# Performance work log

Measured on AMD Instinct MI355X. Metric: run time of the kernel, lower is better.

The kernel has to match this reference:

```python
import jax, jax.numpy as jnp
import numpy as np

LATENT_H = 5
LATENT_W = 5
BN_EPS = 1e-5


def setup_inputs() -> dict:
    key = jax.random.key(0)
    k1, k2 = jax.random.split(key)
    B, T, C, H, W = 8, 4, 512, 32, 32
    return {
        "left_features": jax.random.normal(k1, (B, T, C, H, W), dtype=jnp.float32),
        "right_features": jax.random.normal(k2, (B, T, C, H, W), dtype=jnp.float32),
        "bn_gamma": jnp.ones((C,), dtype=jnp.float32),
        "bn_beta": jnp.zeros((C,), dtype=jnp.float32),
    }


def _batchnorm_per_t(x, gamma, beta):
    # x: (B, T, C, H, W); train-mode BN applied independently at each timestep
    # (stats over batch + spatial dims, per channel, per t)
    mu = jnp.mean(x, axis=(0, 3, 4), keepdims=True)          # (1, T, C, 1, 1)
    var = jnp.var(x, axis=(0, 3, 4), keepdims=True)
    g = gamma[None, None, :, None, None]
    b = beta[None, None, :, None, None]
    return (x - mu) * jax.lax.rsqrt(var + BN_EPS) * g + b


def reference(left_features, right_features, bn_gamma, bn_beta):
    l = _batchnorm_per_t(left_features, bn_gamma, bn_beta)
    r = _batchnorm_per_t(right_features, bn_gamma, bn_beta)
    # channel-summed squared difference: (B, T, H, W)
    diff2 = jnp.sum((l - r) ** 2, axis=2)
    # latent_h x latent_w windowed mean, stride 1, VALID -> (B, T, Hp, Wp)
    win_sum = jax.lax.reduce_window(
        diff2, 0.0, jax.lax.add,
        window_dimensions=(1, 1, LATENT_H, LATENT_W),
        window_strides=(1, 1, 1, 1),
        padding="VALID",
    )
    heatmap = jnp.sqrt(win_sum / (LATENT_H * LATENT_W))
    B, T, Hp, Wp = heatmap.shape
    flat = heatmap.reshape(B, T, Hp * Wp)
    asymmetry_values = jnp.max(flat, axis=-1)                # (B, T)
    idx = jnp.argmin(flat, axis=-1)                          # (B, T)
    x_argmin = idx % Wp
    y_argmin = idx // Wp
    asymmetry_coords = jnp.stack([x_argmin, y_argmin], axis=-1)  # (B, T, 2)
    return asymmetry_values, asymmetry_coords, heatmap
```

## Files before the change

### kernel.cpp

```cpp
#include <hip/hip_runtime.h>

#define T_ 4
#define C_ 512
#define B_ 8
#define HW_ 1024
#define W_ 32
#define HP_ 28
#define EPS_ 1e-5f
#define CCH 16
#define NCHUNK (C_ / CCH)

__global__ __launch_bounds__(256) void stats_kernel(const float* __restrict__ L,
                                                    const float* __restrict__ R,
                                                    const float* __restrict__ gamma,
                                                    float4* __restrict__ coef) {
    const int tc = blockIdx.x;
    const int tid = threadIdx.x;
    const int t = tc >> 9;
    const int c = tc & (C_ - 1);
    const float4* L4 = (const float4*)L;
    const float4* R4 = (const float4*)R;

    float sl = 0.f, ql = 0.f, sr = 0.f, qr = 0.f;
#pragma unroll
    for (int b = 0; b < B_; ++b) {
        size_t base4 = ((size_t)(b * T_ + t) * C_ + c) * (HW_ / 4);
        float4 vl = L4[base4 + tid];
        float4 vr = R4[base4 + tid];
        sl += vl.x + vl.y + vl.z + vl.w;
        ql += vl.x * vl.x + vl.y * vl.y + vl.z * vl.z + vl.w * vl.w;
        sr += vr.x + vr.y + vr.z + vr.w;
        qr += vr.x * vr.x + vr.y * vr.y + vr.z * vr.z + vr.w * vr.w;
    }

#pragma unroll
    for (int off = 32; off > 0; off >>= 1) {
        sl += __shfl_down(sl, off);
        ql += __shfl_down(ql, off);
        sr += __shfl_down(sr, off);
        qr += __shfl_down(qr, off);
    }

    __shared__ float red[4][4];
    const int wave = tid >> 6, lane = tid & 63;
    if (lane == 0) {
        red[0][wave] = sl; red[1][wave] = ql;
        red[2][wave] = sr; red[3][wave] = qr;
    }
    __syncthreads();
    if (tid == 0) {
        float S  = red[0][0] + red[0][1] + red[0][2] + red[0][3];
        float Q  = red[1][0] + red[1][1] + red[1][2] + red[1][3];
        float Sr = red[2][0] + red[2][1] + red[2][2] + red[2][3];
        float Qr = red[3][0] + red[3][1] + red[3][2] + red[3][3];
        const float inv = 1.0f / (float)(B_ * HW_);
        float mul = S * inv, mur = Sr * inv;
        float varl = Q * inv - mul * mul;
        float varr = Qr * inv - mur * mur;
        float s_l = rsqrtf(varl + EPS_);
        float s_r = rsqrtf(varr + EPS_);
        float g = gamma[c];
        coef[tc] = make_float4(g * s_l, g * s_r, g * (s_l * mul - s_r * mur), 0.f);
    }
}

__global__ __launch_bounds__(256) void diff2_kernel(const float* __restrict__ L,
                                                    const float* __restrict__ R,
                                                    const float4* __restrict__ coef,
                                                    float4* __restrict__ part4) {
    const int chunk = blockIdx.x;
    const int bt = blockIdx.y;
    const int t = bt & (T_ - 1);
    const int tid = threadIdx.x;
    const int c0 = chunk * CCH;

    __shared__ float4 cf[CCH];
    if (tid < CCH) cf[tid] = coef[t * C_ + c0 + tid];
    __syncthreads();

    const float4* L4 = (const float4*)L;
    const float4* R4 = (const float4*)R;
    const size_t base4 = ((size_t)bt * C_ + c0) * (HW_ / 4);

    float a0 = 0.f, a1 = 0.f, a2 = 0.f, a3 = 0.f;
#pragma unroll
    for (int cc = 0; cc < CCH; ++cc) {
        float4 k = cf[cc];
        float4 vl = L4[base4 + cc * (HW_ / 4) + tid];
        float4 vr = R4[base4 + cc * (HW_ / 4) + tid];
        float d0 = k.x * vl.x - k.y * vr.x - k.z;
        float d1 = k.x * vl.y - k.y * vr.y - k.z;
        float d2 = k.x * vl.z - k.y * vr.z - k.z;
        float d3 = k.x * vl.w - k.y * vr.w - k.z;
        a0 += d0 * d0; a1 += d1 * d1; a2 += d2 * d2; a3 += d3 * d3;
    }
    part4[((size_t)chunk * (B_ * T_) + bt) * (HW_ / 4) + tid] =
        make_float4(a0, a1, a2, a3);
}

__global__ __launch_bounds__(256) void finalize_kernel(const float4* __restrict__ part4,
                                                       float* __restrict__ out) {
    const int bt = blockIdx.x;
    const int tid = threadIdx.x;
    __shared__ float d[HW_];
    __shared__ float rowsum[32][HP_];
    __shared__ float rv[256];
    __shared__ int   ri[256];
    __shared__ float rmax[256];

    float4 s = make_float4(0.f, 0.f, 0.f, 0.f);
#pragma unroll
    for (int ch = 0; ch < NCHUNK; ++ch) {
        float4 v = part4[((size_t)ch * (B_ * T_) + bt) * (HW_ / 4) + tid];
        s.x += v.x; s.y += v.y; s.z += v.z; s.w += v.w;
    }
    ((float4*)d)[tid] = s;
    __syncthreads();

    for (int i = tid; i < 32 * HP_; i += 256) {
        int h = i / HP_, w = i % HP_;
        const float* row = d + h * W_ + w;
        rowsum[h][w] = row[0] + row[1] + row[2] + row[3] + row[4];
    }
    __syncthreads();

    float lmax = -1e30f, lmin = 1e30f;
    int lidx = 0;
    for (int i = tid; i < HP_ * HP_; i += 256) {
        int hh = i / HP_, w = i % HP_;
        float ws = rowsum[hh][w] + rowsum[hh + 1][w] + rowsum[hh + 2][w] +
                   rowsum[hh + 3][w] + rowsum[hh + 4][w];
        float hm = sqrtf(ws * (1.0f / 25.0f));
        out[96 + (size_t)bt * (HP_ * HP_) + i] = hm;
        lmax = fmaxf(lmax, hm);
        if (hm < lmin) { lmin = hm; lidx = i; }
    }
    rv[tid] = lmin; ri[tid] = lidx; rmax[tid] = lmax;
    __syncthreads();
    for (int st = 128; st > 0; st >>= 1) {
        if (tid < st) {
            float ov = rv[tid + st]; int oi = ri[tid + st];
            if (ov < rv[tid] || (ov == rv[tid] && oi < ri[tid])) { rv[tid] = ov; ri[tid] = oi; }
            rmax[tid] = fmaxf(rmax[tid], rmax[tid + st]);
        }
        __syncthreads();
    }
    if (tid == 0) {
        out[bt] = rmax[0];
        int idx = ri[0];
        out[32 + 2 * bt + 0] = (float)(idx % HP_);
        out[32 + 2 * bt + 1] = (float)(idx / HP_);
    }
}

extern "C" void kernel_launch(void* const* d_in, const int* in_sizes, int n_in,
                              void* d_out, int out_size, void* d_ws, size_t ws_size,
                              hipStream_t stream) {
    const float* L = (const float*)d_in[0];
    const float* R = (const float*)d_in[1];
    const float* gamma = (const float*)d_in[2];
    float* out = (float*)d_out;

    float4* coef = (float4*)d_ws;
    float4* part4 = (float4*)((char*)d_ws + 4 * sizeof(float4) * (T_ * C_) / 4 * 4);
    part4 = (float4*)((char*)d_ws + sizeof(float4) * (T_ * C_));

    stats_kernel<<<T_ * C_, 256, 0, stream>>>(L, R, gamma, coef);
    diff2_kernel<<<dim3(NCHUNK, B_ * T_), 256, 0, stream>>>(L, R, coef, part4);
    finalize_kernel<<<B_ * T_, 256, 0, stream>>>(part4, out);
}
```

Baseline: 171.4 us.

## Split BN stats per row into wave-level partials and fold finalize into diff2

The stats kernel now assigns one wave to each (b,t,c) row and writes per-row partial sums, replacing one block per (t,c) that strided across the batch. The diff2 kernel reduces those partials over the batch and computes the BN coefficients in shared memory before its main loop. That main loop is also unrolled by four channels so more loads are in flight. The aim is contiguous per-wave memory access and more loads in flight for these bandwidth-bound passes, in exchange for a small redundant coefficient computation in every diff2 block.

```diff
diff --git a/kernel.cpp b/kernel.cpp
--- a/kernel.cpp
+++ b/kernel.cpp
@@ -9,29 +9,40 @@
 #define EPS_ 1e-5f
 #define CCH 16
 #define NCHUNK (C_ / CCH)
+#define NBT (B_ * T_)
+#define NROWS (B_ * T_ * C_)
 
 __global__ __launch_bounds__(256) void stats_kernel(const float* __restrict__ L,
                                                     const float* __restrict__ R,
-                                                    const float* __restrict__ gamma,
-                                                    float4* __restrict__ coef) {
-    const int tc = blockIdx.x;
-    const int tid = threadIdx.x;
-    const int t = tc >> 9;
-    const int c = tc & (C_ - 1);
+                                                    float4* __restrict__ part_s) {
+    const int wave = threadIdx.x >> 6;
+    const int lane = threadIdx.x & 63;
+    const int row = blockIdx.x * 4 + wave;
     const float4* L4 = (const float4*)L;
     const float4* R4 = (const float4*)R;
-
-    float sl = 0.f, ql = 0.f, sr = 0.f, qr = 0.f;
-#pragma unroll
-    for (int b = 0; b < B_; ++b) {
-        size_t base4 = ((size_t)(b * T_ + t) * C_ + c) * (HW_ / 4);
-        float4 vl = L4[base4 + tid];
-        float4 vr = R4[base4 + tid];
-        sl += vl.x + vl.y + vl.z + vl.w;
-        ql += vl.x * vl.x + vl.y * vl.y + vl.z * vl.z + vl.w * vl.w;
-        sr += vr.x + vr.y + vr.z + vr.w;
-        qr += vr.x * vr.x + vr.y * vr.y + vr.z * vr.z + vr.w * vr.w;
-    }
+    const size_t base = (size_t)row * 256 + lane;
+
+    float4 l0 = L4[base      ];
+    float4 l1 = L4[base +  64];
+    float4 l2 = L4[base + 128];
+    float4 l3 = L4[base + 192];
+    float4 r0 = R4[base      ];
+    float4 r1 = R4[base +  64];
+    float4 r2 = R4[base + 128];
+    float4 r3 = R4[base + 192];
+
+    float sl = (l0.x + l0.y + l0.z + l0.w) + (l1.x + l1.y + l1.z + l1.w)
+             + (l2.x + l2.y + l2.z + l2.w) + (l3.x + l3.y + l3.z + l3.w);
+    float ql = (l0.x*l0.x + l0.y*l0.y + l0.z*l0.z + l0.w*l0.w)
+             + (l1.x*l1.x + l1.y*l1.y + l1.z*l1.z + l1.w*l1.w)
+             + (l2.x*l2.x + l2.y*l2.y + l2.z*l2.z + l2.w*l2.w)
+             + (l3.x*l3.x + l3.y*l3.y + l3.z*l3.z + l3.w*l3.w);
+    float sr = (r0.x + r0.y + r0.z + r0.w) + (r1.x + r1.y + r1.z + r1.w)
+             + (r2.x + r2.y + r2.z + r2.w) + (r3.x + r3.y + r3.z + r3.w);
+    float qr = (r0.x*r0.x + r0.y*r0.y + r0.z*r0.z + r0.w*r0.w)
+             + (r1.x*r1.x + r1.y*r1.y + r1.z*r1.z + r1.w*r1.w)
+             + (r2.x*r2.x + r2.y*r2.y + r2.z*r2.z + r2.w*r2.w)
+             + (r3.x*r3.x + r3.y*r3.y + r3.z*r3.z + r3.w*r3.w);
 
 #pragma unroll
     for (int off = 32; off > 0; off >>= 1) {
@@ -40,42 +51,44 @@
         sr += __shfl_down(sr, off);
         qr += __shfl_down(qr, off);
     }
-
-    __shared__ float red[4][4];
-    const int wave = tid >> 6, lane = tid & 63;
-    if (lane == 0) {
-        red[0][wave] = sl; red[1][wave] = ql;
-        red[2][wave] = sr; red[3][wave] = qr;
-    }
-    __syncthreads();
-    if (tid == 0) {
-        float S  = red[0][0] + red[0][1] + red[0][2] + red[0][3];
-        float Q  = red[1][0] + red[1][1] + red[1][2] + red[1][3];
-        float Sr = red[2][0] + red[2][1] + red[2][2] + red[2][3];
-        float Qr = red[3][0] + red[3][1] + red[3][2] + red[3][3];
+    if (lane == 0) part_s[row] = make_float4(sl, ql, sr, qr);
+}
+
+__global__ __launch_bounds__(256) void diff2_kernel(const float* __restrict__ L,
+                                                    const float* __restrict__ R,
+                                                    const float4* __restrict__ part_s,
+                                                    const float* __restrict__ gamma,
+                                                    float4* __restrict__ part4) {
+    const int chunk = blockIdx.x;
+    const int bt = blockIdx.y;
+    const int t = bt & (T_ - 1);
+    const int tid = threadIdx.x;
+    const int c0 = chunk * CCH;
+
+    __shared__ float4 spart[B_][CCH];
+    __shared__ float4 cf[CCH];
+
+    if (tid < B_ * CCH) {
+        int bg = tid >> 4, ci = tid & (CCH - 1);
+        spart[bg][ci] = part_s[(bg * T_ + t) * C_ + c0 + ci];
+    }
+    __syncthreads();
+    if (tid < CCH) {
+        float S = 0.f, Q = 0.f, Sr = 0.f, Qr = 0.f;
+#pragma unroll
+        for (int bg = 0; bg < B_; ++bg) {
+            float4 v = spart[bg][tid];
+            S += v.x; Q += v.y; Sr += v.z; Qr += v.w;
+        }
         const float inv = 1.0f / (float)(B_ * HW_);
         float mul = S * inv, mur = Sr * inv;
         float varl = Q * inv - mul * mul;
         float varr = Qr * inv - mur * mur;
         float s_l = rsqrtf(varl + EPS_);
         float s_r = rsqrtf(varr + EPS_);
-        float g = gamma[c];
-        coef[tc] = make_float4(g * s_l, g * s_r, g * (s_l * mul - s_r * mur), 0.f);
-    }
-}
-
-__global__ __launch_bounds__(256) void diff2_kernel(const float* __restrict__ L,
-                                                    const float* __restrict__ R,
-                                                    const float4* __restrict__ coef,
-                                                    float4* __restrict__ part4) {
-    const int chunk = blockIdx.x;
-    const int bt = blockIdx.y;
-    const int t = bt & (T_ - 1);
-    const int tid = threadIdx.x;
-    const int c0 = chunk * CCH;
-
-    __shared__ float4 cf[CCH];
-    if (tid < CCH) cf[tid] = coef[t * C_ + c0 + tid];
+        float g = gamma[c0 + tid];
+        cf[tid] = make_float4(g * s_l, g * s_r, g * (s_l * mul - s_r * mur), 0.f);
+    }
     __syncthreads();
 
     const float4* L4 = (const float4*)L;
@@ -84,18 +97,35 @@
 
     float a0 = 0.f, a1 = 0.f, a2 = 0.f, a3 = 0.f;
 #pragma unroll
-    for (int cc = 0; cc < CCH; ++cc) {
-        float4 k = cf[cc];
-        float4 vl = L4[base4 + cc * (HW_ / 4) + tid];
-        float4 vr = R4[base4 + cc * (HW_ / 4) + tid];
-        float d0 = k.x * vl.x - k.y * vr.x - k.z;
-        float d1 = k.x * vl.y - k.y * vr.y - k.z;
-        float d2 = k.x * vl.z - k.y * vr.z - k.z;
-        float d3 = k.x * vl.w - k.y * vr.w - k.z;
-        a0 += d0 * d0; a1 += d1 * d1; a2 += d2 * d2; a3 += d3 * d3;
-    }
-    part4[((size_t)chunk * (B_ * T_) + bt) * (HW_ / 4) + tid] =
-        make_float4(a0, a1, a2, a3);
+    for (int cc = 0; cc < CCH; cc += 4) {
+        float4 vl0 = L4[base4 + (cc + 0) * (HW_ / 4) + tid];
+        float4 vl1 = L4[base4 + (cc + 1) * (HW_ / 4) + tid];
+        float4 vl2 = L4[base4 + (cc + 2) * (HW_ / 4) + tid];
+        float4 vl3 = L4[base4 + (cc + 3) * (HW_ / 4) + tid];
+        float4 vr0 = R4[base4 + (cc + 0) * (HW_ / 4) + tid];
+        float4 vr1 = R4[base4 + (cc + 1) * (HW_ / 4) + tid];
+        float4 vr2 = R4[base4 + (cc + 2) * (HW_ / 4) + tid];
+        float4 vr3 = R4[base4 + (cc + 3) * (HW_ / 4) + tid];
+        float4 k0 = cf[cc + 0], k1 = cf[cc + 1], k2 = cf[cc + 2], k3 = cf[cc + 3];
+        float d0, d1, d2, d3;
+        d0 = k0.x*vl0.x - k0.y*vr0.x - k0.z; a0 += d0*d0;
+        d1 = k0.x*vl0.y - k0.y*vr0.y - k0.z; a1 += d1*d1;
+        d2 = k0.x*vl0.z - k0.y*vr0.z - k0.z; a2 += d2*d2;
+        d3 = k0.x*vl0.w - k0.y*vr0.w - k0.z; a3 += d3*d3;
+        d0 = k1.x*vl1.x - k1.y*vr1.x - k1.z; a0 += d0*d0;
+        d1 = k1.x*vl1.y - k1.y*vr1.y - k1.z; a1 += d1*d1;
+        d2 = k1.x*vl1.z - k1.y*vr1.z - k1.z; a2 += d2*d2;
+        d3 = k1.x*vl1.w - k1.y*vr1.w - k1.z; a3 += d3*d3;
+        d0 = k2.x*vl2.x - k2.y*vr2.x - k2.z; a0 += d0*d0;
+        d1 = k2.x*vl2.y - k2.y*vr2.y - k2.z; a1 += d1*d1;
+        d2 = k2.x*vl2.z - k2.y*vr2.z - k2.z; a2 += d2*d2;
+        d3 = k2.x*vl2.w - k2.y*vr2.w - k2.z; a3 += d3*d3;
+        d0 = k3.x*vl3.x - k3.y*vr3.x - k3.z; a0 += d0*d0;
+        d1 = k3.x*vl3.y - k3.y*vr3.y - k3.z; a1 += d1*d1;
+        d2 = k3.x*vl3.z - k3.y*vr3.z - k3.z; a2 += d2*d2;
+        d3 = k3.x*vl3.w - k3.y*vr3.w - k3.z; a3 += d3*d3;
+    }
+    part4[((size_t)chunk * NBT + bt) * (HW_ / 4) + tid] = make_float4(a0, a1, a2, a3);
 }
 
 __global__ __launch_bounds__(256) void finalize_kernel(const float4* __restrict__ part4,
@@ -111,7 +141,7 @@
     float4 s = make_float4(0.f, 0.f, 0.f, 0.f);
 #pragma unroll
     for (int ch = 0; ch < NCHUNK; ++ch) {
-        float4 v = part4[((size_t)ch * (B_ * T_) + bt) * (HW_ / 4) + tid];
+        float4 v = part4[((size_t)ch * NBT + bt) * (HW_ / 4) + tid];
         s.x += v.x; s.y += v.y; s.z += v.z; s.w += v.w;
     }
     ((float4*)d)[tid] = s;
@@ -161,11 +191,10 @@
     const float* gamma = (const float*)d_in[2];
     float* out = (float*)d_out;
 
-    float4* coef = (float4*)d_ws;
-    float4* part4 = (float4*)((char*)d_ws + 4 * sizeof(float4) * (T_ * C_) / 4 * 4);
-    part4 = (float4*)((char*)d_ws + sizeof(float4) * (T_ * C_));
-
-    stats_kernel<<<T_ * C_, 256, 0, stream>>>(L, R, gamma, coef);
-    diff2_kernel<<<dim3(NCHUNK, B_ * T_), 256, 0, stream>>>(L, R, coef, part4);
-    finalize_kernel<<<B_ * T_, 256, 0, stream>>>(part4, out);
-}
+    float4* part_s = (float4*)d_ws;
+    float4* part4 = (float4*)((char*)d_ws + sizeof(float4) * NROWS);
+
+    stats_kernel<<<NROWS / 4, 256, 0, stream>>>(L, R, part_s);
+    diff2_kernel<<<dim3(NCHUNK, NBT), 256, 0, stream>>>(L, R, part_s, gamma, part4);
+    finalize_kernel<<<NBT, 256, 0, stream>>>(part4, out);
+}
```

New measurement: 170.9 us. About the same (-0.3%).
